# Kernel tuning notes

Hardware: AMD Instinct MI355X
Metric: run time of the kernel (lower is better)

## Reference

```python
import jax, jax.numpy as jnp
import numpy as np

N = 100000
E = 1600000
D_IN = 128
D_OUT = 128

def setup_inputs() -> dict:
    key = jax.random.key(0)
    k1, k2, k3, k4, k5, k6 = jax.random.split(key, 6)
    h = jax.random.normal(k1, (N, D_IN), dtype=jnp.float32)
    # norm ~ deg^{-1/2}; use positive uniform values as stand-in
    norm = jax.random.uniform(k2, (N, 1), dtype=jnp.float32, minval=0.05, maxval=1.0)
    src = jax.random.randint(k3, (E,), 0, N, dtype=jnp.int32)
    dst = jax.random.randint(k4, (E,), 0, N, dtype=jnp.int32)
    weight = jax.random.normal(k5, (D_IN, D_OUT), dtype=jnp.float32) * (2.0 / (D_IN + D_OUT)) ** 0.5
    bias = jnp.zeros((D_OUT,), dtype=jnp.float32)
    return {"h": h, "norm": norm, "src": src, "dst": dst, "weight": weight, "bias": bias}

def reference(h, norm, src, dst, weight, bias):
    n_nodes = h.shape[0]
    hw = h @ weight                      # [N, D_out] dense GEMM
    hw = hw * norm                       # pre-aggregation degree scale
    msgs = hw[src]                       # gather: [E, D_out]
    agg = jax.ops.segment_sum(msgs, dst, num_segments=n_nodes)  # scatter-sum
    out = agg * norm + bias              # post-scale + bias
    return out
```

## Files before the change

kernel.cpp:

```cpp
#include <hip/hip_runtime.h>
#include <hip/hip_bf16.h>

#define D 128
#define D4 32
#define CHUNK 3072
#define MAXB 2048
#define NSEG 8
#define SL 4096

typedef __attribute__((ext_vector_type(8))) short bf16x8;
typedef __attribute__((ext_vector_type(8))) unsigned short ushort8;
typedef __attribute__((ext_vector_type(4))) float f32x4;

static __device__ __forceinline__ unsigned short f2bf(float f) {
    unsigned u = __float_as_uint(f);
    u += 0x7FFFu + ((u >> 16) & 1u);
    return (unsigned short)(u >> 16);
}
static __device__ __forceinline__ float bf2f(unsigned short u) {
    return __uint_as_float(((unsigned)u) << 16);
}

__global__ __launch_bounds__(256) void wcvt_kernel(
    const float* __restrict__ W, unsigned short* __restrict__ Wt)
{
    const int idx = blockIdx.x * 256 + threadIdx.x;
    const float4 w = ((const float4*)W)[idx];
    const int k = idx >> 5;
    const int c = (idx & 31) * 4;
    Wt[(c + 0) * 128 + k] = f2bf(w.x);
    Wt[(c + 1) * 128 + k] = f2bf(w.y);
    Wt[(c + 2) * 128 + k] = f2bf(w.z);
    Wt[(c + 3) * 128 + k] = f2bf(w.w);
}

__global__ __launch_bounds__(256) void gemm_mfma_kernel(
    const float* __restrict__ h, const unsigned short* __restrict__ Wt,
    const float* __restrict__ norm, unsigned short* __restrict__ hwb,
    int n_nodes)
{
    __shared__ unsigned short As[64 * 136];
    __shared__ unsigned short Bs[128 * 136];

    const int t = threadIdx.x;
    const int row0 = blockIdx.x * 64;

    #pragma unroll
    for (int i = 0; i < 8; ++i) {
        const int idx = t + 256 * i;
        const int c = idx >> 4;
        const int k8 = idx & 15;
        const ushort8 w = ((const ushort8*)Wt)[idx];
        *(ushort8*)&Bs[c * 136 + k8 * 8] = w;
    }
    #pragma unroll
    for (int i = 0; i < 8; ++i) {
        const int idx = t + 256 * i;
        const int r = idx >> 5;
        const int kq = idx & 31;
        long gr = row0 + r; if (gr >= n_nodes) gr = n_nodes - 1;
        const float4 a = ((const float4*)(h + gr * D))[kq];
        ushort4 o;
        o.x = f2bf(a.x); o.y = f2bf(a.y); o.z = f2bf(a.z); o.w = f2bf(a.w);
        *(ushort4*)&As[r * 136 + kq * 4] = o;
    }
    __syncthreads();

    const int wv = t >> 6;
    const int lane = t & 63;
    const int m = lane & 15;
    const int quad = lane >> 4;

    f32x4 acc[8];
    #pragma unroll
    for (int nt = 0; nt < 8; ++nt) { f32x4 z = {0.f, 0.f, 0.f, 0.f}; acc[nt] = z; }

    #pragma unroll
    for (int kt = 0; kt < 4; ++kt) {
        const bf16x8 af = *(const bf16x8*)&As[(wv * 16 + m) * 136 + kt * 32 + quad * 8];
        #pragma unroll
        for (int nt = 0; nt < 8; ++nt) {
            const bf16x8 bfr = *(const bf16x8*)&Bs[(nt * 16 + m) * 136 + kt * 32 + quad * 8];
            acc[nt] = __builtin_amdgcn_mfma_f32_16x16x32_bf16(af, bfr, acc[nt], 0, 0, 0);
        }
    }

    float nv[4];
    #pragma unroll
    for (int i = 0; i < 4; ++i) {
        const int gr = row0 + wv * 16 + quad * 4 + i;
        nv[i] = (gr < n_nodes) ? norm[gr] : 0.f;
    }
    #pragma unroll
    for (int nt = 0; nt < 8; ++nt) {
        #pragma unroll
        for (int i = 0; i < 4; ++i) {
            const int gr = row0 + wv * 16 + quad * 4 + i;
            if (gr < n_nodes)
                hwb[(size_t)gr * D + nt * 16 + m] = f2bf(acc[nt][i] * nv[i]);
        }
    }
}

__global__ __launch_bounds__(1024) void hist_kernel(
    const int* __restrict__ dst, int* __restrict__ H,
    unsigned short* __restrict__ hwb, int n_edges, int n_nodes)
{
    __shared__ int lbh[MAXB];
    const int t = threadIdx.x;
    const int g = blockIdx.x;
    for (int i = t; i < MAXB; i += 1024) lbh[i] = 0;
    if (g == 0 && t < 32) {
        ushort4 z; z.x = z.y = z.z = z.w = 0;
        ((ushort4*)(hwb + (size_t)n_nodes * D))[t] = z;
    }
    __syncthreads();
    const int e0 = g * CHUNK;
    const int e1 = min(e0 + CHUNK, n_edges);
    for (int e = e0 + t; e < e1; e += 1024) {
        atomicAdd(&lbh[dst[e] >> 6], 1);
    }
    __syncthreads();
    for (int i = t; i < MAXB; i += 1024) {
        H[(size_t)g * MAXB + i] = lbh[i];
    }
}

__global__ __launch_bounds__(256) void colsum_kernel(
    const int* __restrict__ H, int* __restrict__ PS, int eb)
{
    const int col = blockIdx.x * 256 + threadIdx.x;
    const int seg = blockIdx.y;
    const int glen = (eb + NSEG - 1) / NSEG;
    const int g0 = seg * glen;
    const int g1 = min(g0 + glen, eb);
    int s = 0;
    for (int g = g0; g < g1; ++g) s += H[(size_t)g * MAXB + col];
    PS[seg * MAXB + col] = s;
}

__global__ __launch_bounds__(256) void bucket_scan_kernel(
    const int* __restrict__ PS, int* __restrict__ boff, int* __restrict__ bcur)
{
    __shared__ int tmp[256];
    const int t = threadIdx.x;
    int v[8];
    int s = 0;
    #pragma unroll
    for (int k = 0; k < 8; ++k) {
        const int i = t * 8 + k;
        int c = 0;
        #pragma unroll
        for (int sg = 0; sg < NSEG; ++sg) c += PS[sg * MAXB + i];
        v[k] = c; s += c;
    }
    tmp[t] = s;
    __syncthreads();
    for (int ofs = 1; ofs < 256; ofs <<= 1) {
        int x = (t >= ofs) ? tmp[t - ofs] : 0;
        __syncthreads();
        tmp[t] += x;
        __syncthreads();
    }
    int run = tmp[t] - s;
    #pragma unroll
    for (int k = 0; k < 8; ++k) {
        boff[t * 8 + k] = run;
        bcur[t * 8 + k] = run;
        run += v[k];
    }
    if (t == 255) boff[MAXB] = run;
}

__global__ __launch_bounds__(1024) void bscatter_kernel(
    const int* __restrict__ src, const int* __restrict__ dst,
    const int* __restrict__ H, int* __restrict__ bcur,
    unsigned int* __restrict__ ebuf, int n_edges)
{
    __shared__ int lbh[MAXB];
    __shared__ int lofs[MAXB];
    const int t = threadIdx.x;
    const int g = blockIdx.x;
    for (int i = t; i < MAXB; i += 1024) {
        lbh[i] = 0;
        const int c = H[(size_t)g * MAXB + i];
        lofs[i] = c ? atomicAdd(&bcur[i], c) : 0;
    }
    __syncthreads();
    const int e0 = g * CHUNK;
    const int e1 = min(e0 + CHUNK, n_edges);
    for (int e = e0 + t; e < e1; e += 1024) {
        const int d = dst[e];
        const int bk = d >> 6;
        const int r = atomicAdd(&lbh[bk], 1);
        ebuf[lofs[bk] + r] = (unsigned)src[e] | ((unsigned)(d & 63) << 17);
    }
}

__global__ __launch_bounds__(256) void fillagg_kernel(
    const unsigned int* __restrict__ ebuf, const int* __restrict__ boff,
    int* __restrict__ srcs_g, const unsigned short* __restrict__ hwb,
    const float* __restrict__ norm, const float* __restrict__ bias,
    float* __restrict__ out, int n_nodes)
{
    __shared__ int slds[SL];
    __shared__ int lcnt[64];
    __shared__ int lcur[64];
    __shared__ int loff[64];
    const int t = threadIdx.x;
    const int b = blockIdx.x;
    const int gn0 = b * 64;

    if (t < 64) lcnt[t] = 0;
    __syncthreads();
    const int w0 = boff[b], w1 = boff[b + 1];
    const int wlen = w1 - w0;
    const bool uselds = (wlen + 480) <= SL;
    const int gbase = w0 + 448 * b;

    for (int e = w0 + t; e < w1; e += 256) {
        atomicAdd(&lcnt[(ebuf[e] >> 17) & 63], 1);
    }
    __syncthreads();
    if (t < 64) {
        const int c = lcnt[t];
        const int p = (c + 7) & ~7;
        int x = p;
        #pragma unroll
        for (int ofs = 1; ofs < 64; ofs <<= 1) {
            const int y = __shfl_up(x, ofs, 64);
            if (t >= ofs) x += y;
        }
        const int base = x - p;
        lcur[t] = base;
        loff[t] = base;
    }
    __syncthreads();
    for (int e = w0 + t; e < w1; e += 256) {
        const unsigned rec = ebuf[e];
        const int loc = (rec >> 17) & 63;
        const int pos = atomicAdd(&lcur[loc], 1);
        const int sv = (int)(rec & 0x1FFFFu);
        if (uselds) slds[pos] = sv; else srcs_g[gbase + pos] = sv;
    }
    for (int w = t; w < 512; w += 256) {
        const int ln = w >> 3, k = w & 7;
        const int gn = gn0 + ln;
        if (gn < n_nodes) {
            const int c = lcnt[ln];
            const int pad = (8 - (c & 7)) & 7;
            if (k < pad) {
                const int pos = loff[ln] + c + k;
                if (uselds) slds[pos] = n_nodes; else srcs_g[gbase + pos] = n_nodes;
            }
        }
    }
    __syncthreads();

    const ushort4* hw4 = (const ushort4*)hwb;
    const int grp = t >> 5;
    const int l = t & 31;
    const float4 bs = ((const float4*)bias)[l];
    for (int nn = 0; nn < 8; ++nn) {
        const int loc = grp * 8 + nn;
        const int gn = gn0 + loc;
        if (gn >= n_nodes) continue;
        const int start = loff[loc];
        const int deg = lcnt[loc];
        const int nb8 = (deg + 7) >> 3;
        float4 acc; acc.x = acc.y = acc.z = acc.w = 0.f;
        int myidx = 0;
        for (int bb = 0; bb < nb8; ++bb) {
            const int q = bb & 3;
            if (q == 0) {
                const int ri = start + bb * 8 + l;
                myidx = uselds ? slds[ri] : srcs_g[gbase + ri];
            }
            ushort4 v[8];
            #pragma unroll
            for (int jj = 0; jj < 8; ++jj) {
                const int s = __shfl(myidx, q * 8 + jj, 32);
                v[jj] = hw4[(long)s * D4 + l];
            }
            #pragma unroll
            for (int jj = 0; jj < 8; ++jj) {
                acc.x += bf2f(v[jj].x);
                acc.y += bf2f(v[jj].y);
                acc.z += bf2f(v[jj].z);
                acc.w += bf2f(v[jj].w);
            }
        }
        const float nv = norm[gn];
        float4 o;
        o.x = acc.x * nv + bs.x;
        o.y = acc.y * nv + bs.y;
        o.z = acc.z * nv + bs.z;
        o.w = acc.w * nv + bs.w;
        ((float4*)out)[(long)gn * D4 + l] = o;
    }
}

__global__ __launch_bounds__(256) void scatter_kernel(
    const unsigned short* __restrict__ hwb, const int* __restrict__ src,
    const int* __restrict__ dst, float* __restrict__ out, int n_edges)
{
    const int idx = blockIdx.x * 256 + threadIdx.x;
    if (idx >= n_edges * D4) return;
    const int e = idx >> 5;
    const int g = idx & 31;
    const int s = src[e];
    const int d = dst[e];
    const ushort4 v = ((const ushort4*)hwb)[(long)s * D4 + g];
    float* o = out + (long)d * D + g * 4;
    atomicAdd(o + 0, bf2f(v.x));
    atomicAdd(o + 1, bf2f(v.y));
    atomicAdd(o + 2, bf2f(v.z));
    atomicAdd(o + 3, bf2f(v.w));
}

__global__ __launch_bounds__(256) void finalize_kernel(
    float* __restrict__ out, const float* __restrict__ norm,
    const float* __restrict__ bias, int n_nodes)
{
    const int idx = blockIdx.x * 256 + threadIdx.x;
    if (idx >= n_nodes * D4) return;
    const int n = idx >> 5;
    const int g = idx & 31;
    float4 v = ((float4*)out)[idx];
    const float nv = norm[n];
    const float4 b = ((const float4*)bias)[g];
    v.x = v.x * nv + b.x;
    v.y = v.y * nv + b.y;
    v.z = v.z * nv + b.z;
    v.w = v.w * nv + b.w;
    ((float4*)out)[idx] = v;
}

extern "C" void kernel_launch(void* const* d_in, const int* in_sizes, int n_in,
                              void* d_out, int out_size, void* d_ws, size_t ws_size,
                              hipStream_t stream) {
    const float* h    = (const float*)d_in[0];
    const float* norm = (const float*)d_in[1];
    const int*   src  = (const int*)d_in[2];
    const int*   dst  = (const int*)d_in[3];
    const float* W    = (const float*)d_in[4];
    const float* bias = (const float*)d_in[5];
    float* out = (float*)d_out;

    const int n_nodes = in_sizes[1];
    const int n_edges = in_sizes[2];

    const int NBUCK = (n_nodes + 63) >> 6;
    const int EB    = (n_edges + CHUNK - 1) / CHUNK;
    const int srcs_len = n_edges + 448 * NBUCK + 64;

    size_t p = 0;
    auto take = [&](size_t bytes) {
        size_t cur = p;
        p += (bytes + 255) & ~(size_t)255;
        return cur;
    };
    const size_t hwb_off  = take(((size_t)n_nodes + 1) * D * sizeof(unsigned short));
    const size_t wt_off   = take((size_t)D * D * sizeof(unsigned short));
    const size_t srcs_off = take((size_t)srcs_len * sizeof(int));
    const size_t ebuf_off = take((size_t)n_edges * sizeof(unsigned int));
    const size_t boff_off = take((MAXB + 1) * sizeof(int));
    const size_t bcur_off = take(MAXB * sizeof(int));
    const size_t H_off    = take((size_t)EB * MAXB * sizeof(int));
    const size_t PS_off   = take((size_t)NSEG * MAXB * sizeof(int));
    const size_t needed = p;

    char* ws = (char*)d_ws;
    unsigned short* hwb = (unsigned short*)(ws + hwb_off);
    unsigned short* Wt  = (unsigned short*)(ws + wt_off);

    wcvt_kernel<<<16, 256, 0, stream>>>(W, Wt);
    gemm_mfma_kernel<<<(n_nodes + 63) / 64, 256, 0, stream>>>(h, Wt, norm, hwb, n_nodes);

    if (ws_size >= needed && NBUCK <= MAXB && n_nodes <= 131072 && EB <= 1024) {
        int* srcs  = (int*)(ws + srcs_off);
        unsigned int* ebuf = (unsigned int*)(ws + ebuf_off);
        int* boff  = (int*)(ws + boff_off);
        int* bcur  = (int*)(ws + bcur_off);
        int* H     = (int*)(ws + H_off);
        int* PS    = (int*)(ws + PS_off);

        hist_kernel<<<EB, 1024, 0, stream>>>(dst, H, hwb, n_edges, n_nodes);
        colsum_kernel<<<dim3(MAXB / 256, NSEG), 256, 0, stream>>>(H, PS, EB);
        bucket_scan_kernel<<<1, 256, 0, stream>>>(PS, boff, bcur);
        bscatter_kernel<<<EB, 1024, 0, stream>>>(src, dst, H, bcur, ebuf, n_edges);
        fillagg_kernel<<<NBUCK, 256, 0, stream>>>(ebuf, boff, srcs, hwb, norm, bias,
                                                  out, n_nodes);
    } else {
        hipMemsetAsync(d_out, 0, (size_t)out_size * sizeof(float), stream);
        const int work = n_edges * D4;
        scatter_kernel<<<(work + 255) / 256, 256, 0, stream>>>(hwb, src, dst, out, n_edges);
        const int work2 = n_nodes * D4;
        finalize_kernel<<<(work2 + 255) / 256, 256, 0, stream>>>(out, norm, bias, n_nodes);
    }
}
```

Baseline: 250.8 us.

## Replace atomic bucket offsets with deterministic chunk scan; stream GEMM A-operand from global

Bucket offsets for each edge chunk were claimed with global atomics on a shared cursor. They are now computed by a segmented prefix scan over the per-chunk histograms, done in a new chunkscan kernel, so bscatter reads precomputed offsets. This removes atomic contention and makes edge ordering deterministic, at the cost of an extra kernel launch and an extra EB x MAXB offset array. The GEMM also drops its shared-memory A tile and has each lane load and convert h directly from global memory. It now uses 128-row, 512-thread blocks, which cuts LDS use and the sync before compute.

```diff
diff --git a/kernel.cpp b/kernel.cpp
--- a/kernel.cpp
+++ b/kernel.cpp
@@ -34,35 +34,22 @@
     Wt[(c + 3) * 128 + k] = f2bf(w.w);
 }
 
-__global__ __launch_bounds__(256) void gemm_mfma_kernel(
+__global__ __launch_bounds__(512) void gemm_mfma_kernel(
     const float* __restrict__ h, const unsigned short* __restrict__ Wt,
     const float* __restrict__ norm, unsigned short* __restrict__ hwb,
     int n_nodes)
 {
-    __shared__ unsigned short As[64 * 136];
     __shared__ unsigned short Bs[128 * 136];
 
     const int t = threadIdx.x;
-    const int row0 = blockIdx.x * 64;
-
-    #pragma unroll
-    for (int i = 0; i < 8; ++i) {
-        const int idx = t + 256 * i;
+    const int row0 = blockIdx.x * 128;
+
+    #pragma unroll
+    for (int i = 0; i < 4; ++i) {
+        const int idx = t + 512 * i;
         const int c = idx >> 4;
         const int k8 = idx & 15;
-        const ushort8 w = ((const ushort8*)Wt)[idx];
-        *(ushort8*)&Bs[c * 136 + k8 * 8] = w;
-    }
-    #pragma unroll
-    for (int i = 0; i < 8; ++i) {
-        const int idx = t + 256 * i;
-        const int r = idx >> 5;
-        const int kq = idx & 31;
-        long gr = row0 + r; if (gr >= n_nodes) gr = n_nodes - 1;
-        const float4 a = ((const float4*)(h + gr * D))[kq];
-        ushort4 o;
-        o.x = f2bf(a.x); o.y = f2bf(a.y); o.z = f2bf(a.z); o.w = f2bf(a.w);
-        *(ushort4*)&As[r * 136 + kq * 4] = o;
+        *(ushort8*)&Bs[c * 136 + k8 * 8] = ((const ushort8*)Wt)[idx];
     }
     __syncthreads();
 
@@ -71,13 +58,22 @@
     const int m = lane & 15;
     const int quad = lane >> 4;
 
+    long gra = row0 + wv * 16 + m;
+    if (gra >= n_nodes) gra = n_nodes - 1;
+    const float* hrow = h + gra * D;
+
     f32x4 acc[8];
     #pragma unroll
     for (int nt = 0; nt < 8; ++nt) { f32x4 z = {0.f, 0.f, 0.f, 0.f}; acc[nt] = z; }
 
     #pragma unroll
     for (int kt = 0; kt < 4; ++kt) {
-        const bf16x8 af = *(const bf16x8*)&As[(wv * 16 + m) * 136 + kt * 32 + quad * 8];
+        const float4 a0 = *(const float4*)(hrow + kt * 32 + quad * 8);
+        const float4 a1 = *(const float4*)(hrow + kt * 32 + quad * 8 + 4);
+        bf16x8 af;
+        unsigned short* ap = (unsigned short*)&af;
+        ap[0] = f2bf(a0.x); ap[1] = f2bf(a0.y); ap[2] = f2bf(a0.z); ap[3] = f2bf(a0.w);
+        ap[4] = f2bf(a1.x); ap[5] = f2bf(a1.y); ap[6] = f2bf(a1.z); ap[7] = f2bf(a1.w);
         #pragma unroll
         for (int nt = 0; nt < 8; ++nt) {
             const bf16x8 bfr = *(const bf16x8*)&Bs[(nt * 16 + m) * 136 + kt * 32 + quad * 8];
@@ -140,7 +136,7 @@
 }
 
 __global__ __launch_bounds__(256) void bucket_scan_kernel(
-    const int* __restrict__ PS, int* __restrict__ boff, int* __restrict__ bcur)
+    const int* __restrict__ PS, int* __restrict__ boff, int* __restrict__ SB)
 {
     __shared__ int tmp[256];
     const int t = threadIdx.x;
@@ -165,16 +161,38 @@
     int run = tmp[t] - s;
     #pragma unroll
     for (int k = 0; k < 8; ++k) {
-        boff[t * 8 + k] = run;
-        bcur[t * 8 + k] = run;
+        const int i = t * 8 + k;
+        boff[i] = run;
+        int sb = run;
+        #pragma unroll
+        for (int sg = 0; sg < NSEG; ++sg) {
+            SB[sg * MAXB + i] = sb;
+            sb += PS[sg * MAXB + i];
+        }
         run += v[k];
     }
     if (t == 255) boff[MAXB] = run;
+}
+
+__global__ __launch_bounds__(256) void chunkscan_kernel(
+    const int* __restrict__ H, const int* __restrict__ SB,
+    int* __restrict__ CO, int eb)
+{
+    const int b = blockIdx.x * 256 + threadIdx.x;
+    const int seg = blockIdx.y;
+    const int glen = (eb + NSEG - 1) / NSEG;
+    const int g0 = seg * glen;
+    const int g1 = min(g0 + glen, eb);
+    int run = SB[seg * MAXB + b];
+    for (int g = g0; g < g1; ++g) {
+        CO[(size_t)g * MAXB + b] = run;
+        run += H[(size_t)g * MAXB + b];
+    }
 }
 
 __global__ __launch_bounds__(1024) void bscatter_kernel(
     const int* __restrict__ src, const int* __restrict__ dst,
-    const int* __restrict__ H, int* __restrict__ bcur,
+    const int* __restrict__ CO,
     unsigned int* __restrict__ ebuf, int n_edges)
 {
     __shared__ int lbh[MAXB];
@@ -183,8 +201,7 @@
     const int g = blockIdx.x;
     for (int i = t; i < MAXB; i += 1024) {
         lbh[i] = 0;
-        const int c = H[(size_t)g * MAXB + i];
-        lofs[i] = c ? atomicAdd(&bcur[i], c) : 0;
+        lofs[i] = CO[(size_t)g * MAXB + i];
     }
     __syncthreads();
     const int e0 = g * CHUNK;
@@ -365,9 +382,10 @@
     const size_t srcs_off = take((size_t)srcs_len * sizeof(int));
     const size_t ebuf_off = take((size_t)n_edges * sizeof(unsigned int));
     const size_t boff_off = take((MAXB + 1) * sizeof(int));
-    const size_t bcur_off = take(MAXB * sizeof(int));
     const size_t H_off    = take((size_t)EB * MAXB * sizeof(int));
     const size_t PS_off   = take((size_t)NSEG * MAXB * sizeof(int));
+    const size_t SB_off   = take((size_t)NSEG * MAXB * sizeof(int));
+    const size_t CO_off   = take((size_t)EB * MAXB * sizeof(int));
     const size_t needed = p;
 
     char* ws = (char*)d_ws;
@@ -375,20 +393,22 @@
     unsigned short* Wt  = (unsigned short*)(ws + wt_off);
 
     wcvt_kernel<<<16, 256, 0, stream>>>(W, Wt);
-    gemm_mfma_kernel<<<(n_nodes + 63) / 64, 256, 0, stream>>>(h, Wt, norm, hwb, n_nodes);
+    gemm_mfma_kernel<<<(n_nodes + 127) / 128, 512, 0, stream>>>(h, Wt, norm, hwb, n_nodes);
 
     if (ws_size >= needed && NBUCK <= MAXB && n_nodes <= 131072 && EB <= 1024) {
         int* srcs  = (int*)(ws + srcs_off);
         unsigned int* ebuf = (unsigned int*)(ws + ebuf_off);
         int* boff  = (int*)(ws + boff_off);
-        int* bcur  = (int*)(ws + bcur_off);
         int* H     = (int*)(ws + H_off);
         int* PS    = (int*)(ws + PS_off);
+        int* SBp   = (int*)(ws + SB_off);
+        int* CO    = (int*)(ws + CO_off);
 
         hist_kernel<<<EB, 1024, 0, stream>>>(dst, H, hwb, n_edges, n_nodes);
         colsum_kernel<<<dim3(MAXB / 256, NSEG), 256, 0, stream>>>(H, PS, EB);
-        bucket_scan_kernel<<<1, 256, 0, stream>>>(PS, boff, bcur);
-        bscatter_kernel<<<EB, 1024, 0, stream>>>(src, dst, H, bcur, ebuf, n_edges);
+        bucket_scan_kernel<<<1, 256, 0, stream>>>(PS, boff, SBp);
+        chunkscan_kernel<<<dim3(MAXB / 256, NSEG), 256, 0, stream>>>(H, SBp, CO, EB);
+        bscatter_kernel<<<EB, 1024, 0, stream>>>(src, dst, CO, ebuf, n_edges);
         fillagg_kernel<<<NBUCK, 256, 0, stream>>>(ebuf, boff, srcs, hwb, norm, bias,
                                                   out, n_nodes);
     } else {
```

Result: no change. 247.1 us (-1.5%).
